# Kernel tuning notes

Measured on AMD Instinct MI355X. Metric: run time of the kernel, lower is better.

Reference implementation:

```python
import jax, jax.numpy as jnp
import numpy as np

NUM_EMB = 1024
EMB_DIM = 256
BETA = 0.25


def setup_inputs() -> dict:
    key = jax.random.key(0)
    k1, k2 = jax.random.split(key)
    z_e = jax.random.normal(k1, (32, EMB_DIM, 32, 32), dtype=jnp.float32)
    # original inits uniform(-1/num_emb, 1/num_emb)
    emb_weight = jax.random.uniform(k2, (NUM_EMB, EMB_DIM), dtype=jnp.float32,
                                    minval=-1.0 / NUM_EMB, maxval=1.0 / NUM_EMB)
    return {"z_e": z_e, "emb_weight": emb_weight}


def reference(z_e, emb_weight):
    # (B, C, H, W) -> (B, H, W, C)
    z = jnp.transpose(z_e, (0, 2, 3, 1))
    B, H, W, C = z.shape
    z_flat = z.reshape(-1, C)  # (N, C)
    # squared L2 distances to codebook: ||z||^2 + ||e||^2 - 2 z e^T
    d = (jnp.sum(z_flat ** 2, axis=1, keepdims=True)
         + jnp.sum(emb_weight ** 2, axis=1)
         - 2.0 * jnp.matmul(z_flat, emb_weight.T))  # (N, num_emb)
    encoding_indices = jnp.argmin(d, axis=1)  # (N,)
    # one-hot matmul == gather of codebook rows
    z_q = jnp.take(emb_weight, encoding_indices, axis=0).reshape(B, H, W, C)
    # vq losses
    L_e = jnp.mean((jax.lax.stop_gradient(z_q) - z) ** 2)
    L_q = jnp.mean((z_q - jax.lax.stop_gradient(z)) ** 2)
    vq_loss = L_e + BETA * L_q
    # straight-through estimator
    z_q_st = z + jax.lax.stop_gradient(z_q - z)
    z_q_out = jnp.transpose(z_q_st, (0, 3, 1, 2))  # (B, C, H, W)
    return z_q_out, vq_loss, encoding_indices
```

## Files before the change

kernel.cpp:

```cpp
#include <hip/hip_runtime.h>

#define NUM_EMB 1024
#define EMB_DIM 256
#define NPIX    32768
#define HW      1024
#define ZQ_ELEMS 8388608

#define WS_TNORM 8
#define WS_SNORM 8192
#define WS_KEYS  139264
#define WS_CNT   401408
#define WS_EPL   401424
#define EPLANE_ELEMS (NUM_EMB * EMB_DIM)

typedef unsigned long long u64;
typedef unsigned int u32;
typedef unsigned short u16;

typedef __bf16 bf16x8 __attribute__((ext_vector_type(8)));
typedef float f32x16 __attribute__((ext_vector_type(16)));
typedef u16 u16x8 __attribute__((ext_vector_type(8)));

__device__ __forceinline__ float pw128_sq(const float* x, int stride) {
  float r[8];
#pragma unroll
  for (int j = 0; j < 8; ++j) {
    float v = x[(size_t)j * stride];
    r[j] = __fmul_rn(v, v);
  }
  for (int i = 8; i < 128; i += 8) {
#pragma unroll
    for (int j = 0; j < 8; ++j) {
      float v = x[(size_t)(i + j) * stride];
      r[j] = __fadd_rn(r[j], __fmul_rn(v, v));
    }
  }
  float s01 = __fadd_rn(r[0], r[1]);
  float s23 = __fadd_rn(r[2], r[3]);
  float s45 = __fadd_rn(r[4], r[5]);
  float s67 = __fadd_rn(r[6], r[7]);
  return __fadd_rn(__fadd_rn(s01, s23), __fadd_rn(s45, s67));
}

__device__ __forceinline__ void split3(float x, u16& h, u16& m, u16& l) {
  u32 u = __float_as_uint(x);
  u16 hb = (u16)((u + 0x7fffu + ((u >> 16) & 1u)) >> 16);
  float hf = __uint_as_float((u32)hb << 16);
  float r1 = x - hf;
  u32 u1 = __float_as_uint(r1);
  u16 mb = (u16)((u1 + 0x7fffu + ((u1 >> 16) & 1u)) >> 16);
  float mf = __uint_as_float((u32)mb << 16);
  float r2 = r1 - mf;
  u32 u2 = __float_as_uint(r2);
  u16 lb = (u16)((u2 + 0x7fffu + ((u2 >> 16) & 1u)) >> 16);
  h = hb; m = mb; l = lb;
}

__device__ __forceinline__ u64 shfl_xor_u64(u64 v, int msk) {
  const u32 lo = __shfl_xor((u32)v, msk, 64);
  const u32 hi = __shfl_xor((u32)(v >> 32), msk, 64);
  return ((u64)hi << 32) | lo;
}

__global__ __launch_bounds__(256) void vq_prep_kernel(
    const float* __restrict__ z, const float* __restrict__ emb,
    float* __restrict__ tnorm, float* __restrict__ snorm,
    u64* __restrict__ keys, double* __restrict__ loss_accum,
    u32* __restrict__ counter,
    u16* __restrict__ eh, u16* __restrict__ em, u16* __restrict__ el) {
  const int gid = blockIdx.x * 256 + threadIdx.x;
  if (gid == 0) *loss_accum = 0.0;
  if (gid == 1) *counter = 0u;
  if (gid < NPIX) {
    keys[gid] = ~0ull;
    const int b = gid >> 10, hw = gid & 1023;
    const float* base = z + (size_t)b * (EMB_DIM * HW) + hw;
    snorm[gid] = __fadd_rn(pw128_sq(base, HW), pw128_sq(base + (size_t)128 * HW, HW));
  } else {
    const int k = gid - NPIX;
    if (k < NUM_EMB) {
      const float* row = emb + (size_t)k * EMB_DIM;
      tnorm[k] = __fadd_rn(pw128_sq(row, 1), pw128_sq(row + 128, 1));
      for (int c = 0; c < EMB_DIM; c += 8) {
        u16x8 vh, vm, vl;
#pragma unroll
        for (int j = 0; j < 8; ++j) {
          u16 h_, m_, l_;
          split3(row[c + j], h_, m_, l_);
          vh[j] = h_; vm[j] = m_; vl[j] = l_;
        }
        *(u16x8*)(eh + (size_t)k * EMB_DIM + c) = vh;
        *(u16x8*)(em + (size_t)k * EMB_DIM + c) = vm;
        *(u16x8*)(el + (size_t)k * EMB_DIM + c) = vl;
      }
    }
  }
}

__global__ __launch_bounds__(256, 2) void vq_main_kernel(
    const float* __restrict__ z,
    const u16* __restrict__ eh, const u16* __restrict__ em,
    const u16* __restrict__ el,
    const float* __restrict__ tnorm, const float* __restrict__ snorm,
    u64* __restrict__ keys) {
  __shared__ __align__(16) u16 zs[3][128][40];
  __shared__ __align__(16) u16 es[3][128][40];

  const int t   = threadIdx.x;
  const int hb  = blockIdx.x;
  const int bid = (hb & 7) * 256 + (hb >> 3);
  const int pt  = bid >> 3;
  const int ntb = bid & 7;
  const int m0  = pt * 128;
  const int n0  = ntb * 128;
  const int b   = m0 >> 10;
  const int hw0 = m0 & 1023;
  const float* zbase = z + (size_t)b * (EMB_DIM * HW) + hw0;

  const int l    = t & 63;
  const int wid  = t >> 6;
  const int wpx0 = (wid >> 1) * 64;
  const int wcb  = (wid & 1) * 64;
  const int cl   = l & 31;
  const int hi   = l >> 5;

  const int sr    = t & 127;
  const int skh   = (t >> 7) * 16;
  const int ecode = t >> 1;
  const int ekh   = (t & 1) * 16;
  const u16* eplan[3] = {eh, em, el};
  const size_t ebase = (size_t)(n0 + ecode) * EMB_DIM + ekh;

  float gz[16];
  u16x8 ge[3][2];

#pragma unroll
  for (int j = 0; j < 16; ++j)
    gz[j] = zbase[(size_t)(skh + j) * HW + sr];
#pragma unroll
  for (int p = 0; p < 3; ++p) {
    ge[p][0] = *(const u16x8*)(eplan[p] + ebase);
    ge[p][1] = *(const u16x8*)(eplan[p] + ebase + 8);
  }

  f32x16 acc[2][2];
#pragma unroll
  for (int i = 0; i < 2; ++i)
#pragma unroll
    for (int j = 0; j < 2; ++j)
#pragma unroll
      for (int r = 0; r < 16; ++r) acc[i][j][r] = 0.0f;

  for (int kt = 0; kt < 8; ++kt) {
#pragma unroll
    for (int c = 0; c < 2; ++c) {
      u16x8 vh, vm, vl;
#pragma unroll
      for (int j = 0; j < 8; ++j) {
        u16 h_, m_, l_;
        split3(gz[c * 8 + j], h_, m_, l_);
        vh[j] = h_; vm[j] = m_; vl[j] = l_;
      }
      *(u16x8*)&zs[0][sr][skh + c * 8] = vh;
      *(u16x8*)&zs[1][sr][skh + c * 8] = vm;
      *(u16x8*)&zs[2][sr][skh + c * 8] = vl;
    }
#pragma unroll
    for (int p = 0; p < 3; ++p) {
      *(u16x8*)&es[p][ecode][ekh]     = ge[p][0];
      *(u16x8*)&es[p][ecode][ekh + 8] = ge[p][1];
    }
    if (kt < 7) {
      const int kb = (kt + 1) * 32;
#pragma unroll
      for (int j = 0; j < 16; ++j)
        gz[j] = zbase[(size_t)(kb + skh + j) * HW + sr];
#pragma unroll
      for (int p = 0; p < 3; ++p) {
        ge[p][0] = *(const u16x8*)(eplan[p] + ebase + kb);
        ge[p][1] = *(const u16x8*)(eplan[p] + ebase + kb + 8);
      }
    }
    __syncthreads();

#pragma unroll
    for (int ks = 0; ks < 2; ++ks) {
      bf16x8 af[3][2], bf[3][2];
#pragma unroll
      for (int p = 0; p < 3; ++p)
#pragma unroll
        for (int mt = 0; mt < 2; ++mt)
          af[p][mt] =
              *(const bf16x8*)&zs[p][wpx0 + mt * 32 + cl][ks * 16 + hi * 8];
#pragma unroll
      for (int p = 0; p < 3; ++p)
#pragma unroll
        for (int nn = 0; nn < 2; ++nn)
          bf[p][nn] =
              *(const bf16x8*)&es[p][wcb + nn * 32 + cl][ks * 16 + hi * 8];
#define PROD(PA, PB)                                                          \
      _Pragma("unroll")                                                       \
      for (int mt = 0; mt < 2; ++mt) {                                        \
        _Pragma("unroll")                                                     \
        for (int nn = 0; nn < 2; ++nn)                                        \
          acc[mt][nn] = __builtin_amdgcn_mfma_f32_32x32x16_bf16(              \
              af[PA][mt], bf[PB][nn], acc[mt][nn], 0, 0, 0);                  \
      }
      PROD(0, 0)
      PROD(0, 1)
      PROD(1, 0)
      PROD(1, 1)
      PROD(0, 2)
      PROD(2, 0)
#undef PROD
    }
    __syncthreads();
  }

  const float tv0 = tnorm[n0 + wcb + cl];
  const float tv1 = tnorm[n0 + wcb + 32 + cl];
  u64 bk[2][16];
#pragma unroll
  for (int mt = 0; mt < 2; ++mt)
#pragma unroll
    for (int reg = 0; reg < 16; ++reg) {
      const int row = wpx0 + mt * 32 + (reg & 3) + 8 * (reg >> 2) + 4 * hi;
      const float s = snorm[m0 + row];
      const float d0 = __fsub_rn(__fadd_rn(s, tv0), 2.0f * acc[mt][0][reg]);
      const float d1 = __fsub_rn(__fadd_rn(s, tv1), 2.0f * acc[mt][1][reg]);
      const u64 k0 = ((u64)__float_as_uint(d0) << 32) | (u32)(n0 + wcb + cl);
      const u64 k1 =
          ((u64)__float_as_uint(d1) << 32) | (u32)(n0 + wcb + 32 + cl);
      bk[mt][reg] = k0 < k1 ? k0 : k1;
    }
#pragma unroll
  for (int off = 1; off < 32; off <<= 1) {
#pragma unroll
    for (int mt = 0; mt < 2; ++mt)
#pragma unroll
      for (int reg = 0; reg < 16; ++reg) {
        const u64 o = shfl_xor_u64(bk[mt][reg], off);
        if (o < bk[mt][reg]) bk[mt][reg] = o;
      }
  }

  u64* part = (u64*)&zs[0][0][0];
  if (cl == 0) {
#pragma unroll
    for (int mt = 0; mt < 2; ++mt)
#pragma unroll
      for (int reg = 0; reg < 16; ++reg) {
        const int row = wpx0 + mt * 32 + (reg & 3) + 8 * (reg >> 2) + 4 * hi;
        part[row * 2 + (wid & 1)] = bk[mt][reg];
      }
  }
  __syncthreads();
  if (t < 128) {
    const u64 a = part[t * 2], c = part[t * 2 + 1];
    atomicMin(&keys[m0 + t], a < c ? a : c);
  }
}

__global__ __launch_bounds__(256) void vq_outputs_kernel(
    const float* __restrict__ z, const float* __restrict__ emb,
    const u64* __restrict__ keys, float* __restrict__ out,
    float* __restrict__ out_idx_f, double* __restrict__ loss_accum,
    u32* __restrict__ counter, float* __restrict__ out_loss) {
  const int t  = threadIdx.x;
  const int n0 = blockIdx.x * 64;
  const int m  = t & 63;
  const int c0 = t >> 6;
  const int b  = n0 >> 10;
  const int hw = n0 & 1023;
  const float* zb = z   + (size_t)b * (EMB_DIM * HW) + hw + m;
  float*       ob = out + (size_t)b * (EMB_DIM * HW) + hw + m;
  const int idx = (int)(u32)(keys[n0 + m] & 0xffffffffu);
  const float* er = emb + (size_t)idx * EMB_DIM;
  if (c0 == 0) out_idx_f[n0 + m] = (float)idx;

  double lsum = 0.0;
  for (int c = c0; c < EMB_DIM; c += 4) {
    const float e  = er[c];
    const float zv = zb[(size_t)c * HW];
    const float diff = e - zv;
    const float zq   = zv + diff;
    ob[(size_t)c * HW] = zq;
    lsum += (double)diff * (double)diff;
  }

  __shared__ double red[256];
  red[t] = lsum;
  __syncthreads();
  for (int s2 = 128; s2 > 0; s2 >>= 1) {
    if (t < s2) red[t] += red[t + s2];
    __syncthreads();
  }
  if (t == 0) {
    atomicAdd(loss_accum, red[0]);
    __threadfence();
    const u32 tick = atomicAdd(counter, 1u);
    if (tick == (u32)(NPIX / 64 - 1)) {
      const double total = atomicAdd(loss_accum, 0.0);
      const float L = (float)(total / (double)ZQ_ELEMS);
      out_loss[0] = __fadd_rn(L, __fmul_rn(0.25f, L));
    }
  }
}

extern "C" void kernel_launch(void* const* d_in, const int* in_sizes, int n_in,
                              void* d_out, int out_size, void* d_ws, size_t ws_size,
                              hipStream_t stream) {
  const float* z   = (const float*)d_in[0];
  const float* emb = (const float*)d_in[1];

  float* out       = (float*)d_out;
  float* out_loss  = out + ZQ_ELEMS;
  float* out_idx_f = out + ZQ_ELEMS + 1;

  double* loss_accum = (double*)d_ws;
  float*  tnorm = (float*)((char*)d_ws + WS_TNORM);
  float*  snorm = (float*)((char*)d_ws + WS_SNORM);
  u64*    keys  = (u64*)((char*)d_ws + WS_KEYS);
  u32*    counter = (u32*)((char*)d_ws + WS_CNT);
  u16* eh = (u16*)((char*)d_ws + WS_EPL);
  u16* em = eh + EPLANE_ELEMS;
  u16* el = em + EPLANE_ELEMS;

  vq_prep_kernel<<<132, 256, 0, stream>>>(z, emb, tnorm, snorm, keys, loss_accum,
                                          counter, eh, em, el);
  vq_main_kernel<<<2048, 256, 0, stream>>>(z, eh, em, el, tnorm, snorm, keys);
  vq_outputs_kernel<<<NPIX / 64, 256, 0, stream>>>(z, emb, keys, out, out_idx_f,
                                                   loss_accum, counter, out_loss);
}
```

Before: 204.1 us.

## Double-buffer LDS tiles, tile-ordered codebook layout, 512-thread blocks in VQ main kernel

The main distance kernel now uses double-buffered shared-memory tiles so that staging the next K-slice overlaps the MFMA work on the current one. This removes one of the two barriers per iteration. The prep kernel writes the bf16 split codebook in a tile-major layout, so each block's codebook loads are contiguous per k-step. Blocks grow to 512 threads (8 waves, each owning a 64x32 output tile), with a 4-way partial argmin reduction. This doubles shared-memory use and limits occupancy to one block per launch bound, which may reduce latency hiding.

```diff
diff --git a/kernel.cpp b/kernel.cpp
--- a/kernel.cpp
+++ b/kernel.cpp
@@ -10,8 +10,7 @@
 #define WS_SNORM 8192
 #define WS_KEYS  139264
 #define WS_CNT   401408
-#define WS_EPL   401424
-#define EPLANE_ELEMS (NUM_EMB * EMB_DIM)
+#define WS_EG    401424
 
 typedef unsigned long long u64;
 typedef unsigned int u32;
@@ -66,8 +65,7 @@
     const float* __restrict__ z, const float* __restrict__ emb,
     float* __restrict__ tnorm, float* __restrict__ snorm,
     u64* __restrict__ keys, double* __restrict__ loss_accum,
-    u32* __restrict__ counter,
-    u16* __restrict__ eh, u16* __restrict__ em, u16* __restrict__ el) {
+    u32* __restrict__ counter, u16* __restrict__ eG) {
   const int gid = blockIdx.x * 256 + threadIdx.x;
   if (gid == 0) *loss_accum = 0.0;
   if (gid == 1) *counter = 0u;
@@ -81,7 +79,9 @@
     if (k < NUM_EMB) {
       const float* row = emb + (size_t)k * EMB_DIM;
       tnorm[k] = __fadd_rn(pw128_sq(row, 1), pw128_sq(row + 128, 1));
-      for (int c = 0; c < EMB_DIM; c += 8) {
+      const int nt = k >> 7, er = k & 127;
+      for (int c8 = 0; c8 < 32; ++c8) {
+        const int c = c8 * 8, kt = c8 >> 2, qq = c8 & 3;
         u16x8 vh, vm, vl;
 #pragma unroll
         for (int j = 0; j < 8; ++j) {
@@ -89,22 +89,22 @@
           split3(row[c + j], h_, m_, l_);
           vh[j] = h_; vm[j] = m_; vl[j] = l_;
         }
-        *(u16x8*)(eh + (size_t)k * EMB_DIM + c) = vh;
-        *(u16x8*)(em + (size_t)k * EMB_DIM + c) = vm;
-        *(u16x8*)(el + (size_t)k * EMB_DIM + c) = vl;
+        u16* dst = eG + ((((size_t)(nt * 8 + kt) * 3 + 0) * 4 + qq) * 128 + er) * 8;
+        *(u16x8*)(dst)                 = vh;
+        *(u16x8*)(dst + 4096)          = vm;
+        *(u16x8*)(dst + 8192)          = vl;
       }
     }
   }
 }
 
-__global__ __launch_bounds__(256, 2) void vq_main_kernel(
-    const float* __restrict__ z,
-    const u16* __restrict__ eh, const u16* __restrict__ em,
-    const u16* __restrict__ el,
+__global__ __launch_bounds__(512, 1) void vq_main_kernel(
+    const float* __restrict__ z, const u16* __restrict__ eG,
     const float* __restrict__ tnorm, const float* __restrict__ snorm,
     u64* __restrict__ keys) {
-  __shared__ __align__(16) u16 zs[3][128][40];
-  __shared__ __align__(16) u16 es[3][128][40];
+  __shared__ __align__(16) u16 zs[2][3][128][40];
+  __shared__ __align__(16) u16 es[2][3][128][40];
+  __shared__ u64 part[128][4];
 
   const int t   = threadIdx.x;
   const int hb  = blockIdx.x;
@@ -119,93 +119,79 @@
 
   const int l    = t & 63;
   const int wid  = t >> 6;
-  const int wpx0 = (wid >> 1) * 64;
-  const int wcb  = (wid & 1) * 64;
+  const int wpx0 = (wid >> 2) * 64;
+  const int wcb  = (wid & 3) * 32;
   const int cl   = l & 31;
   const int hi   = l >> 5;
 
-  const int sr    = t & 127;
-  const int skh   = (t >> 7) * 16;
-  const int ecode = t >> 1;
-  const int ekh   = (t & 1) * 16;
-  const u16* eplan[3] = {eh, em, el};
-  const size_t ebase = (size_t)(n0 + ecode) * EMB_DIM + ekh;
-
-  float gz[16];
-  u16x8 ge[3][2];
-
-#pragma unroll
-  for (int j = 0; j < 16; ++j)
-    gz[j] = zbase[(size_t)(skh + j) * HW + sr];
-#pragma unroll
-  for (int p = 0; p < 3; ++p) {
-    ge[p][0] = *(const u16x8*)(eplan[p] + ebase);
-    ge[p][1] = *(const u16x8*)(eplan[p] + ebase + 8);
-  }
-
-  f32x16 acc[2][2];
+  const int sr = t & 127;
+  const int q  = t >> 7;
+
+  float gz[8];
+  u16x8 ge[3];
+
+  auto load_z = [&](int kt) {
+#pragma unroll
+    for (int j = 0; j < 8; ++j)
+      gz[j] = zbase[(size_t)(kt * 32 + q * 8 + j) * HW + sr];
+  };
+  auto load_e = [&](int kt) {
+#pragma unroll
+    for (int p = 0; p < 3; ++p)
+      ge[p] = *(const u16x8*)(eG +
+          ((((size_t)(ntb * 8 + kt) * 3 + p) * 4 + q) * 128 + sr) * 8);
+  };
+  auto stage = [&](int buf) {
+    u16x8 vh, vm, vl;
+#pragma unroll
+    for (int j = 0; j < 8; ++j) {
+      u16 h_, m_, l_;
+      split3(gz[j], h_, m_, l_);
+      vh[j] = h_; vm[j] = m_; vl[j] = l_;
+    }
+    *(u16x8*)&zs[buf][0][sr][q * 8] = vh;
+    *(u16x8*)&zs[buf][1][sr][q * 8] = vm;
+    *(u16x8*)&zs[buf][2][sr][q * 8] = vl;
+#pragma unroll
+    for (int p = 0; p < 3; ++p)
+      *(u16x8*)&es[buf][p][sr][q * 8] = ge[p];
+  };
+
+  f32x16 acc[2];
 #pragma unroll
   for (int i = 0; i < 2; ++i)
 #pragma unroll
-    for (int j = 0; j < 2; ++j)
-#pragma unroll
-      for (int r = 0; r < 16; ++r) acc[i][j][r] = 0.0f;
-
+    for (int r = 0; r < 16; ++r) acc[i][r] = 0.0f;
+
+  load_z(0); load_e(0);
+  stage(0);
+  load_z(1); load_e(1);
+  asm volatile("s_waitcnt lgkmcnt(0)" ::: "memory");
+  __builtin_amdgcn_s_barrier();
+
+#pragma unroll 2
   for (int kt = 0; kt < 8; ++kt) {
-#pragma unroll
-    for (int c = 0; c < 2; ++c) {
-      u16x8 vh, vm, vl;
-#pragma unroll
-      for (int j = 0; j < 8; ++j) {
-        u16 h_, m_, l_;
-        split3(gz[c * 8 + j], h_, m_, l_);
-        vh[j] = h_; vm[j] = m_; vl[j] = l_;
+    const int cur = kt & 1;
+    if (kt < 7) {
+      stage(cur ^ 1);
+      if (kt < 6) { load_z(kt + 2); load_e(kt + 2); }
+    }
+#pragma unroll
+    for (int ks = 0; ks < 2; ++ks) {
+      bf16x8 af[3][2], bf[3];
+#pragma unroll
+      for (int p = 0; p < 3; ++p) {
+#pragma unroll
+        for (int mt = 0; mt < 2; ++mt)
+          af[p][mt] = *(const bf16x8*)
+              &zs[cur][p][wpx0 + mt * 32 + cl][ks * 16 + hi * 8];
+        bf[p] = *(const bf16x8*)&es[cur][p][wcb + cl][ks * 16 + hi * 8];
       }
-      *(u16x8*)&zs[0][sr][skh + c * 8] = vh;
-      *(u16x8*)&zs[1][sr][skh + c * 8] = vm;
-      *(u16x8*)&zs[2][sr][skh + c * 8] = vl;
-    }
-#pragma unroll
-    for (int p = 0; p < 3; ++p) {
-      *(u16x8*)&es[p][ecode][ekh]     = ge[p][0];
-      *(u16x8*)&es[p][ecode][ekh + 8] = ge[p][1];
-    }
-    if (kt < 7) {
-      const int kb = (kt + 1) * 32;
-#pragma unroll
-      for (int j = 0; j < 16; ++j)
-        gz[j] = zbase[(size_t)(kb + skh + j) * HW + sr];
-#pragma unroll
-      for (int p = 0; p < 3; ++p) {
-        ge[p][0] = *(const u16x8*)(eplan[p] + ebase + kb);
-        ge[p][1] = *(const u16x8*)(eplan[p] + ebase + kb + 8);
-      }
-    }
-    __syncthreads();
-
-#pragma unroll
-    for (int ks = 0; ks < 2; ++ks) {
-      bf16x8 af[3][2], bf[3][2];
-#pragma unroll
-      for (int p = 0; p < 3; ++p)
-#pragma unroll
-        for (int mt = 0; mt < 2; ++mt)
-          af[p][mt] =
-              *(const bf16x8*)&zs[p][wpx0 + mt * 32 + cl][ks * 16 + hi * 8];
-#pragma unroll
-      for (int p = 0; p < 3; ++p)
-#pragma unroll
-        for (int nn = 0; nn < 2; ++nn)
-          bf[p][nn] =
-              *(const bf16x8*)&es[p][wcb + nn * 32 + cl][ks * 16 + hi * 8];
 #define PROD(PA, PB)                                                          \
-      _Pragma("unroll")                                                       \
-      for (int mt = 0; mt < 2; ++mt) {                                        \
-        _Pragma("unroll")                                                     \
-        for (int nn = 0; nn < 2; ++nn)                                        \
-          acc[mt][nn] = __builtin_amdgcn_mfma_f32_32x32x16_bf16(              \
-              af[PA][mt], bf[PB][nn], acc[mt][nn], 0, 0, 0);                  \
-      }
+      acc[0] = __builtin_amdgcn_mfma_f32_32x32x16_bf16(af[PA][0], bf[PB],     \
+                                                       acc[0], 0, 0, 0);      \
+      acc[1] = __builtin_amdgcn_mfma_f32_32x32x16_bf16(af[PA][1], bf[PB],     \
+                                                       acc[1], 0, 0, 0);
       PROD(0, 0)
       PROD(0, 1)
       PROD(1, 0)
@@ -214,11 +200,13 @@
       PROD(2, 0)
 #undef PROD
     }
-    __syncthreads();
-  }
-
-  const float tv0 = tnorm[n0 + wcb + cl];
-  const float tv1 = tnorm[n0 + wcb + 32 + cl];
+    if (kt < 7) {
+      asm volatile("s_waitcnt lgkmcnt(0)" ::: "memory");
+      __builtin_amdgcn_s_barrier();
+    }
+  }
+
+  const float tv = tnorm[n0 + wcb + cl];
   u64 bk[2][16];
 #pragma unroll
   for (int mt = 0; mt < 2; ++mt)
@@ -226,12 +214,9 @@
     for (int reg = 0; reg < 16; ++reg) {
       const int row = wpx0 + mt * 32 + (reg & 3) + 8 * (reg >> 2) + 4 * hi;
       const float s = snorm[m0 + row];
-      const float d0 = __fsub_rn(__fadd_rn(s, tv0), 2.0f * acc[mt][0][reg]);
-      const float d1 = __fsub_rn(__fadd_rn(s, tv1), 2.0f * acc[mt][1][reg]);
-      const u64 k0 = ((u64)__float_as_uint(d0) << 32) | (u32)(n0 + wcb + cl);
-      const u64 k1 =
-          ((u64)__float_as_uint(d1) << 32) | (u32)(n0 + wcb + 32 + cl);
-      bk[mt][reg] = k0 < k1 ? k0 : k1;
+      const float d = __fsub_rn(__fadd_rn(s, tv), 2.0f * acc[mt][reg]);
+      bk[mt][reg] =
+          ((u64)__float_as_uint(d) << 32) | (u32)(n0 + wcb + cl);
     }
 #pragma unroll
   for (int off = 1; off < 32; off <<= 1) {
@@ -244,20 +229,24 @@
       }
   }
 
-  u64* part = (u64*)&zs[0][0][0];
   if (cl == 0) {
 #pragma unroll
     for (int mt = 0; mt < 2; ++mt)
 #pragma unroll
       for (int reg = 0; reg < 16; ++reg) {
         const int row = wpx0 + mt * 32 + (reg & 3) + 8 * (reg >> 2) + 4 * hi;
-        part[row * 2 + (wid & 1)] = bk[mt][reg];
+        part[row][wid & 3] = bk[mt][reg];
       }
   }
   __syncthreads();
   if (t < 128) {
-    const u64 a = part[t * 2], c = part[t * 2 + 1];
-    atomicMin(&keys[m0 + t], a < c ? a : c);
+    u64 best = part[t][0];
+#pragma unroll
+    for (int x = 1; x < 4; ++x) {
+      const u64 o = part[t][x];
+      if (o < best) best = o;
+    }
+    atomicMin(&keys[m0 + t], best);
   }
 }
 
@@ -322,13 +311,11 @@
   float*  snorm = (float*)((char*)d_ws + WS_SNORM);
   u64*    keys  = (u64*)((char*)d_ws + WS_KEYS);
   u32*    counter = (u32*)((char*)d_ws + WS_CNT);
-  u16* eh = (u16*)((char*)d_ws + WS_EPL);
-  u16* em = eh + EPLANE_ELEMS;
-  u16* el = em + EPLANE_ELEMS;
+  u16*    eG    = (u16*)((char*)d_ws + WS_EG);
 
   vq_prep_kernel<<<132, 256, 0, stream>>>(z, emb, tnorm, snorm, keys, loss_accum,
-                                          counter, eh, em, el);
-  vq_main_kernel<<<2048, 256, 0, stream>>>(z, eh, em, el, tnorm, snorm, keys);
+                                          counter, eG);
+  vq_main_kernel<<<2048, 512, 0, stream>>>(z, eG, tnorm, snorm, keys);
   vq_outputs_kernel<<<NPIX / 64, 256, 0, stream>>>(z, emb, keys, out, out_idx_f,
                                                    loss_accum, counter, out_loss);
 }
```

After: 238.5 us. 1.17x slower.

## Pre-swizzle codebook planes into MFMA fragment order and drop block-level barriers

Applied to the files above, without the earlier changes.

The prep kernel now writes the bf16 hi/mid/lo codebook planes in an MFMA-fragment-ordered layout, so the main kernel loads B operands straight from global memory into registers instead of staging them through shared memory. Each wave stages only its own 64-pixel slice of z in a private LDS region, which removes the per-k-tile __syncthreads barriers, and B fragments are double-buffered across the two k-substeps. This is meant to cut LDS traffic and synchronisation stalls. In exchange each wave re-reads codebook fragments from global/L2 with no sharing across waves, and register pressure goes up.

```diff
diff --git a/kernel.cpp b/kernel.cpp
--- a/kernel.cpp
+++ b/kernel.cpp
@@ -10,8 +10,7 @@
 #define WS_SNORM 8192
 #define WS_KEYS  139264
 #define WS_CNT   401408
-#define WS_EPL   401424
-#define EPLANE_ELEMS (NUM_EMB * EMB_DIM)
+#define WS_EB    403456
 
 typedef unsigned long long u64;
 typedef unsigned int u32;
@@ -20,6 +19,11 @@
 typedef __bf16 bf16x8 __attribute__((ext_vector_type(8)));
 typedef float f32x16 __attribute__((ext_vector_type(16)));
 typedef u16 u16x8 __attribute__((ext_vector_type(8)));
+
+__device__ __forceinline__ size_t eb_idx(int p, int g, int kt, int ks, int hi,
+                                         int cl) {
+  return ((((((size_t)p * 32 + g) * 8 + kt) * 2 + ks) * 2 + hi) * 32 + cl) * 8;
+}
 
 __device__ __forceinline__ float pw128_sq(const float* x, int stride) {
   float r[8];
@@ -66,8 +70,7 @@
     const float* __restrict__ z, const float* __restrict__ emb,
     float* __restrict__ tnorm, float* __restrict__ snorm,
     u64* __restrict__ keys, double* __restrict__ loss_accum,
-    u32* __restrict__ counter,
-    u16* __restrict__ eh, u16* __restrict__ em, u16* __restrict__ el) {
+    u32* __restrict__ counter, u16* __restrict__ EB) {
   const int gid = blockIdx.x * 256 + threadIdx.x;
   if (gid == 0) *loss_accum = 0.0;
   if (gid == 1) *counter = 0u;
@@ -81,6 +84,7 @@
     if (k < NUM_EMB) {
       const float* row = emb + (size_t)k * EMB_DIM;
       tnorm[k] = __fadd_rn(pw128_sq(row, 1), pw128_sq(row + 128, 1));
+      const int g = k >> 5, cl = k & 31;
       for (int c = 0; c < EMB_DIM; c += 8) {
         u16x8 vh, vm, vl;
 #pragma unroll
@@ -89,22 +93,21 @@
           split3(row[c + j], h_, m_, l_);
           vh[j] = h_; vm[j] = m_; vl[j] = l_;
         }
-        *(u16x8*)(eh + (size_t)k * EMB_DIM + c) = vh;
-        *(u16x8*)(em + (size_t)k * EMB_DIM + c) = vm;
-        *(u16x8*)(el + (size_t)k * EMB_DIM + c) = vl;
+        const int kt = c >> 5, ks = (c >> 4) & 1, hi = (c >> 3) & 1;
+        *(u16x8*)(EB + eb_idx(0, g, kt, ks, hi, cl)) = vh;
+        *(u16x8*)(EB + eb_idx(1, g, kt, ks, hi, cl)) = vm;
+        *(u16x8*)(EB + eb_idx(2, g, kt, ks, hi, cl)) = vl;
       }
     }
   }
 }
 
 __global__ __launch_bounds__(256, 2) void vq_main_kernel(
-    const float* __restrict__ z,
-    const u16* __restrict__ eh, const u16* __restrict__ em,
-    const u16* __restrict__ el,
+    const float* __restrict__ z, const u16* __restrict__ EB,
     const float* __restrict__ tnorm, const float* __restrict__ snorm,
     u64* __restrict__ keys) {
-  __shared__ __align__(16) u16 zs[3][128][40];
-  __shared__ __align__(16) u16 es[3][128][40];
+  __shared__ __align__(16) u16 zs[4][3][64][40];
+  __shared__ u64 part[128][2];
 
   const int t   = threadIdx.x;
   const int hb  = blockIdx.x;
@@ -115,7 +118,6 @@
   const int n0  = ntb * 128;
   const int b   = m0 >> 10;
   const int hw0 = m0 & 1023;
-  const float* zbase = z + (size_t)b * (EMB_DIM * HW) + hw0;
 
   const int l    = t & 63;
   const int wid  = t >> 6;
@@ -123,25 +125,46 @@
   const int wcb  = (wid & 1) * 64;
   const int cl   = l & 31;
   const int hi   = l >> 5;
-
-  const int sr    = t & 127;
-  const int skh   = (t >> 7) * 16;
-  const int ecode = t >> 1;
-  const int ekh   = (t & 1) * 16;
-  const u16* eplan[3] = {eh, em, el};
-  const size_t ebase = (size_t)(n0 + ecode) * EMB_DIM + ekh;
-
-  float gz[16];
-  u16x8 ge[3][2];
-
-#pragma unroll
-  for (int j = 0; j < 16; ++j)
-    gz[j] = zbase[(size_t)(skh + j) * HW + sr];
-#pragma unroll
-  for (int p = 0; p < 3; ++p) {
-    ge[p][0] = *(const u16x8*)(eplan[p] + ebase);
-    ge[p][1] = *(const u16x8*)(eplan[p] + ebase + 8);
-  }
+  const int gb   = ntb * 4 + (wid & 1) * 2;
+
+  const int m_ = l & 31;
+  const int h_ = l >> 5;
+  const float* zcol = z + (size_t)b * (EMB_DIM * HW) + hw0 + wpx0 + 2 * m_;
+
+  float2 gz[16];
+  bf16x8 geA[3][2], geB[3][2];
+
+  auto load_gz = [&](int kt) {
+#pragma unroll
+    for (int j = 0; j < 16; ++j)
+      gz[j] = *(const float2*)(zcol + (size_t)(kt * 32 + h_ * 16 + j) * HW);
+  };
+  auto load_ge = [&](bf16x8 dst[3][2], int kt, int ks) {
+#pragma unroll
+    for (int p = 0; p < 3; ++p)
+#pragma unroll
+      for (int nn = 0; nn < 2; ++nn)
+        dst[p][nn] = *(const bf16x8*)(EB + eb_idx(p, gb + nn, kt, ks, hi, cl));
+  };
+  auto stage = [&]() {
+#pragma unroll
+    for (int r = 0; r < 2; ++r) {
+#pragma unroll
+      for (int c = 0; c < 2; ++c) {
+        u16x8 vh, vm, vl;
+#pragma unroll
+        for (int j = 0; j < 8; ++j) {
+          const float x = r ? gz[c * 8 + j].y : gz[c * 8 + j].x;
+          u16 h3, m3, l3;
+          split3(x, h3, m3, l3);
+          vh[j] = h3; vm[j] = m3; vl[j] = l3;
+        }
+        *(u16x8*)&zs[wid][0][2 * m_ + r][h_ * 16 + c * 8] = vh;
+        *(u16x8*)&zs[wid][1][2 * m_ + r][h_ * 16 + c * 8] = vm;
+        *(u16x8*)&zs[wid][2][2 * m_ + r][h_ * 16 + c * 8] = vl;
+      }
+    }
+  };
 
   f32x16 acc[2][2];
 #pragma unroll
@@ -151,70 +174,55 @@
 #pragma unroll
       for (int r = 0; r < 16; ++r) acc[i][j][r] = 0.0f;
 
+  load_gz(0);
+  load_ge(geA, 0, 0);
+  stage();
+  load_gz(1);
+
   for (int kt = 0; kt < 8; ++kt) {
-#pragma unroll
-    for (int c = 0; c < 2; ++c) {
-      u16x8 vh, vm, vl;
-#pragma unroll
-      for (int j = 0; j < 8; ++j) {
-        u16 h_, m_, l_;
-        split3(gz[c * 8 + j], h_, m_, l_);
-        vh[j] = h_; vm[j] = m_; vl[j] = l_;
-      }
-      *(u16x8*)&zs[0][sr][skh + c * 8] = vh;
-      *(u16x8*)&zs[1][sr][skh + c * 8] = vm;
-      *(u16x8*)&zs[2][sr][skh + c * 8] = vl;
-    }
-#pragma unroll
-    for (int p = 0; p < 3; ++p) {
-      *(u16x8*)&es[p][ecode][ekh]     = ge[p][0];
-      *(u16x8*)&es[p][ecode][ekh + 8] = ge[p][1];
-    }
-    if (kt < 7) {
-      const int kb = (kt + 1) * 32;
-#pragma unroll
-      for (int j = 0; j < 16; ++j)
-        gz[j] = zbase[(size_t)(kb + skh + j) * HW + sr];
-#pragma unroll
-      for (int p = 0; p < 3; ++p) {
-        ge[p][0] = *(const u16x8*)(eplan[p] + ebase + kb);
-        ge[p][1] = *(const u16x8*)(eplan[p] + ebase + kb + 8);
-      }
-    }
-    __syncthreads();
-
-#pragma unroll
-    for (int ks = 0; ks < 2; ++ks) {
-      bf16x8 af[3][2], bf[3][2];
+    load_ge(geB, kt, 1);
+    {
+      bf16x8 af[3][2];
 #pragma unroll
       for (int p = 0; p < 3; ++p)
 #pragma unroll
         for (int mt = 0; mt < 2; ++mt)
-          af[p][mt] =
-              *(const bf16x8*)&zs[p][wpx0 + mt * 32 + cl][ks * 16 + hi * 8];
-#pragma unroll
-      for (int p = 0; p < 3; ++p)
-#pragma unroll
-        for (int nn = 0; nn < 2; ++nn)
-          bf[p][nn] =
-              *(const bf16x8*)&es[p][wcb + nn * 32 + cl][ks * 16 + hi * 8];
-#define PROD(PA, PB)                                                          \
+          af[p][mt] = *(const bf16x8*)&zs[wid][p][mt * 32 + cl][hi * 8];
+#define PROD(PA, PB, GE)                                                      \
       _Pragma("unroll")                                                       \
       for (int mt = 0; mt < 2; ++mt) {                                        \
         _Pragma("unroll")                                                     \
         for (int nn = 0; nn < 2; ++nn)                                        \
           acc[mt][nn] = __builtin_amdgcn_mfma_f32_32x32x16_bf16(              \
-              af[PA][mt], bf[PB][nn], acc[mt][nn], 0, 0, 0);                  \
-      }
-      PROD(0, 0)
-      PROD(0, 1)
-      PROD(1, 0)
-      PROD(1, 1)
-      PROD(0, 2)
-      PROD(2, 0)
+              af[PA][mt], GE[PB][nn], acc[mt][nn], 0, 0, 0);                  \
+      }
+      PROD(0, 0, geA)
+      PROD(0, 1, geA)
+      PROD(1, 0, geA)
+      PROD(1, 1, geA)
+      PROD(0, 2, geA)
+      PROD(2, 0, geA)
+    }
+    if (kt < 7) load_ge(geA, kt + 1, 0);
+    {
+      bf16x8 af[3][2];
+#pragma unroll
+      for (int p = 0; p < 3; ++p)
+#pragma unroll
+        for (int mt = 0; mt < 2; ++mt)
+          af[p][mt] = *(const bf16x8*)&zs[wid][p][mt * 32 + cl][16 + hi * 8];
+      PROD(0, 0, geB)
+      PROD(0, 1, geB)
+      PROD(1, 0, geB)
+      PROD(1, 1, geB)
+      PROD(0, 2, geB)
+      PROD(2, 0, geB)
 #undef PROD
     }
-    __syncthreads();
+    if (kt < 7) {
+      stage();
+      if (kt < 6) load_gz(kt + 2);
+    }
   }
 
   const float tv0 = tnorm[n0 + wcb + cl];
@@ -244,19 +252,18 @@
       }
   }
 
-  u64* part = (u64*)&zs[0][0][0];
   if (cl == 0) {
 #pragma unroll
     for (int mt = 0; mt < 2; ++mt)
 #pragma unroll
       for (int reg = 0; reg < 16; ++reg) {
         const int row = wpx0 + mt * 32 + (reg & 3) + 8 * (reg >> 2) + 4 * hi;
-        part[row * 2 + (wid & 1)] = bk[mt][reg];
+        part[row][wid & 1] = bk[mt][reg];
       }
   }
   __syncthreads();
   if (t < 128) {
-    const u64 a = part[t * 2], c = part[t * 2 + 1];
+    const u64 a = part[t][0], c = part[t][1];
     atomicMin(&keys[m0 + t], a < c ? a : c);
   }
 }
@@ -322,13 +329,11 @@
   float*  snorm = (float*)((char*)d_ws + WS_SNORM);
   u64*    keys  = (u64*)((char*)d_ws + WS_KEYS);
   u32*    counter = (u32*)((char*)d_ws + WS_CNT);
-  u16* eh = (u16*)((char*)d_ws + WS_EPL);
-  u16* em = eh + EPLANE_ELEMS;
-  u16* el = em + EPLANE_ELEMS;
+  u16*    EB    = (u16*)((char*)d_ws + WS_EB);
 
   vq_prep_kernel<<<132, 256, 0, stream>>>(z, emb, tnorm, snorm, keys, loss_accum,
-                                          counter, eh, em, el);
-  vq_main_kernel<<<2048, 256, 0, stream>>>(z, eh, em, el, tnorm, snorm, keys);
+                                          counter, EB);
+  vq_main_kernel<<<2048, 256, 0, stream>>>(z, EB, tnorm, snorm, keys);
   vq_outputs_kernel<<<NPIX / 64, 256, 0, stream>>>(z, emb, keys, out, out_idx_f,
                                                    loss_accum, counter, out_loss);
 }
```

After: 204.5 us. About the same (+0.2%).
